# Kernel tuning notes

Hardware: AMD Instinct MI355X
Metric: run time of the kernel (lower is better)

## Reference

```python
import jax, jax.numpy as jnp
import numpy as np

N = 50000          # nodes
E_RAND = 800000    # random edges (avg degree 16)
D_IN = 128
H = 4              # heads (both layers)
C = 64             # per-head channels (both layers)
NEG_SLOPE = 0.2    # PyG GATConv default leaky_relu slope


def _gat_conv(x, src, dst, W, att_src, att_dst, bias, concat):
    """PyG GATConv (dropout=0, self-loops already in edge list).
    x:[N,Din] W:[Din,H*C] att_*:[H,C] bias:[H*C] or [C]."""
    n = x.shape[0]
    h = (x @ W).reshape(n, H, C)                      # [N,H,C]
    a_src = jnp.sum(h * att_src, axis=-1)             # [N,H]
    a_dst = jnp.sum(h * att_dst, axis=-1)             # [N,H]
    e = jax.nn.leaky_relu(a_src[src] + a_dst[dst], NEG_SLOPE)  # [E,H]
    # segment softmax over incoming edges of each destination node
    m = jax.ops.segment_max(e, dst, num_segments=n)    # [N,H]
    e = jnp.exp(e - m[dst])
    denom = jax.ops.segment_sum(e, dst, num_segments=n)
    alpha = e / (denom[dst] + 1e-16)                   # [E,H]
    msg = h[src] * alpha[..., None]                    # [E,H,C]
    out = jax.ops.segment_sum(msg, dst, num_segments=n)  # [N,H,C]
    if concat:
        out = out.reshape(n, H * C)
    else:
        out = out.mean(axis=1)
    return out + bias


def setup_inputs() -> dict:
    key = jax.random.key(0)
    ks = jax.random.split(key, 10)
    x = jax.random.normal(ks[0], (N, D_IN), jnp.float32)
    src = jax.random.randint(ks[1], (E_RAND,), 0, N)
    dst = jax.random.randint(ks[2], (E_RAND,), 0, N)
    loops = jnp.arange(N)  # add_self_loops=True (PyG default)
    edge_index = jnp.stack([jnp.concatenate([src, loops]),
                            jnp.concatenate([dst, loops])]).astype(jnp.int32)
    g = lambda k, shp, fan: (jax.random.normal(k, shp, jnp.float32) / np.float32(np.sqrt(fan)))
    W1 = g(ks[3], (D_IN, H * C), D_IN)
    att_src1 = g(ks[4], (H, C), C)
    att_dst1 = g(ks[5], (H, C), C)
    b1 = jnp.zeros((H * C,), jnp.float32)
    W2 = g(ks[6], (H * C, H * C), H * C)
    att_src2 = g(ks[7], (H, C), C)
    att_dst2 = g(ks[8], (H, C), C)
    b2 = jnp.zeros((C,), jnp.float32)
    return {"x": x, "edge_index": edge_index,
            "W1": W1, "att_src1": att_src1, "att_dst1": att_dst1, "b1": b1,
            "W2": W2, "att_src2": att_src2, "att_dst2": att_dst2, "b2": b2}


def reference(x, edge_index, W1, att_src1, att_dst1, b1, W2, att_src2, att_dst2, b2):
    src, dst = edge_index[0], edge_index[1]
    h = jax.nn.relu(_gat_conv(x, src, dst, W1, att_src1, att_dst1, b1, concat=True))
    h = jax.nn.relu(_gat_conv(h, src, dst, W2, att_src2, att_dst2, b2, concat=False))
    return jax.nn.softmax(h, axis=1)
```

## Files before the change

### kernel.cpp

```cpp
#include <hip/hip_runtime.h>


typedef __attribute__((ext_vector_type(8))) short short8;
typedef __attribute__((ext_vector_type(4))) float f32x4;
typedef __attribute__((ext_vector_type(2))) float f32x2;

static __device__ __forceinline__ ushort f2bf(float f) {
  uint u = __float_as_uint(f);
  return (ushort)((u + 0x7FFFu + ((u >> 16) & 1u)) >> 16);
}
static __device__ __forceinline__ float bf2f(ushort s) {
  return __uint_as_float(((uint)s) << 16);
}
static __device__ __forceinline__ unsigned char f2fp8(float f) {
  int p = __builtin_amdgcn_cvt_pk_fp8_f32(f, f, 0, false);
  return (unsigned char)(p & 0xFF);
}
static __device__ __forceinline__ uint4 cvt8bf(const float4& a, const float4& b) {
  uint4 hh;
  hh.x = (uint)f2bf(a.x) | ((uint)f2bf(a.y) << 16);
  hh.y = (uint)f2bf(a.z) | ((uint)f2bf(a.w) << 16);
  hh.z = (uint)f2bf(b.x) | ((uint)f2bf(b.y) << 16);
  hh.w = (uint)f2bf(b.z) | ((uint)f2bf(b.w) << 16);
  return hh;
}
static __device__ __forceinline__ void gl16(const ushort* g, ushort* l) {
  __builtin_amdgcn_global_load_lds(
      (const __attribute__((address_space(1))) uint*)(g),
      (__attribute__((address_space(3))) uint*)(l), 16, 0, 0);
}

__global__ __launch_bounds__(256)
void k_prep_hist(const float* __restrict__ W1, const float* __restrict__ W2,
                 ushort* __restrict__ w1th, ushort* __restrict__ w1tl,
                 ushort* __restrict__ w2th, ushort* __restrict__ w2tl,
                 const int* __restrict__ dstv, int* __restrict__ cnt,
                 int* __restrict__ pe, int E,
                 const float* __restrict__ x, ushort* __restrict__ xb,
                 int ng ) {
  const int b = blockIdx.x;
  const int eb = (E + 255) >> 8;
  if (b < 128) {
    int gid = b * 256 + threadIdx.x;
    int c = gid & 255, k = gid >> 8;
    float w = W1[(size_t)k * 256 + c];
    ushort h = f2bf(w);
    w1th[(size_t)c * 128 + k] = h;
    w1tl[(size_t)c * 128 + k] = f2bf(w - bf2f(h));
  } else if (b < 384) {
    int gid = (b - 128) * 256 + threadIdx.x;
    int c = gid & 255, k = gid >> 8;
    float w = W2[(size_t)k * 256 + c];
    ushort h = f2bf(w);
    w2th[(size_t)c * 256 + k] = h;
    w2tl[(size_t)c * 256 + k] = f2bf(w - bf2f(h));
  } else if (b < 384 + eb) {
    int i = (b - 384) * 256 + threadIdx.x;
    if (i < E) pe[i] = atomicAdd(&cnt[dstv[i]], 1);
  } else {
    int i = (b - 384 - eb) * 256 + threadIdx.x;
    if (i < ng) {
      const float4* xp = (const float4*)x + (size_t)i * 2;
      float4 a = xp[0], bb = xp[1];
      ((uint4*)xb)[i] = cvt8bf(a, bb);
    }
  }
}

__global__ __launch_bounds__(256)
void k_scan(const int* __restrict__ cnt, int* __restrict__ rowptr,
            int* __restrict__ bsum, int* __restrict__ bflag, int N, int E) {
  __shared__ int sm[256];
  __shared__ int s_prev;
  const int b = blockIdx.x, tid = threadIdx.x;
  const int gid = b * 256 + tid;
  int v = (gid < N) ? cnt[gid] : 0;
  sm[tid] = v;
  __syncthreads();
  for (int off = 1; off < 256; off <<= 1) {
    int t = (tid >= off) ? sm[tid - off] : 0;
    __syncthreads();
    sm[tid] += t;
    __syncthreads();
  }
  if (tid == 255) {
    atomicExch(&bsum[b], sm[255]);
    __threadfence();
    atomicExch(&bflag[b], 1);
  }
  if (tid == 0) s_prev = 0;
  __syncthreads();
  if (tid < b) {
    while (atomicAdd(&bflag[tid], 0) == 0) {}
    atomicAdd(&s_prev, atomicAdd(&bsum[tid], 0));
  }
  __syncthreads();
  if (gid < N) rowptr[gid] = s_prev + sm[tid] - v;
  if (gid == 0) rowptr[N] = E;
}

template <int K>
static __device__ __forceinline__
void gemm_body(int bid, const ushort* __restrict__ Ah,
               const ushort* __restrict__ Bth, const ushort* __restrict__ Btl,
               unsigned char* __restrict__ hout, int Nrows,
               const float* __restrict__ att_s, const float* __restrict__ att_d,
               float* __restrict__ a_s, float* __restrict__ a_d) {
  __shared__ ushort Asb[2][128][32];
  __shared__ ushort Bhb[2][128][32];
  __shared__ ushort Blb[2][128][32];

  const int nrb = (Nrows + 127) >> 7;
  const int rb = (bid >> 4) * 8 + (bid & 7);
  const int ch = (bid >> 3) & 1;
  if (rb >= nrb) return;
  const int row0 = rb * 128;
  const int col0 = ch * 128;

  const int t = threadIdx.x;
  const int lane = t & 63;
  const int w = t >> 6;
  const int wr = (w >> 1) * 64;
  const int wc = (w & 1) * 64;
  const int fr = lane & 15;
  const int fq = lane >> 4;

  const int srow = lane >> 2;
  const int skc = (lane & 3) * 8;
  int ar0 = row0 + w * 32 + srow;
  int ar1 = ar0 + 16;
  ar0 = ar0 < Nrows ? ar0 : Nrows - 1;
  ar1 = ar1 < Nrows ? ar1 : Nrows - 1;
  const ushort* agp0 = Ah + (size_t)ar0 * K + skc;
  const ushort* agp1 = Ah + (size_t)ar1 * K + skc;
  const ushort* bhg0 = Bth + (size_t)(col0 + w * 32 + srow) * K + skc;
  const ushort* bhg1 = bhg0 + (size_t)16 * K;
  const ushort* blg0 = Btl + (size_t)(col0 + w * 32 + srow) * K + skc;
  const ushort* blg1 = blg0 + (size_t)16 * K;

  f32x4 acc[4][4] = {};

  auto stage = [&](int buf, int k0) {
    gl16(agp0 + k0, &Asb[buf][w * 32][0]);
    gl16(agp1 + k0, &Asb[buf][w * 32 + 16][0]);
    gl16(bhg0 + k0, &Bhb[buf][w * 32][0]);
    gl16(bhg1 + k0, &Bhb[buf][w * 32 + 16][0]);
    gl16(blg0 + k0, &Blb[buf][w * 32][0]);
    gl16(blg1 + k0, &Blb[buf][w * 32 + 16][0]);
  };

  stage(0, 0);
  const int NK = K / 32;
#pragma unroll
  for (int ks = 0; ks < NK; ks++) {
    const int buf = ks & 1;
    __syncthreads();
    if (ks + 1 < NK) stage(buf ^ 1, (ks + 1) * 32);

    short8 fa[4], fbh[4], fbl[4];
#pragma unroll
    for (int r = 0; r < 4; r++)
      fa[r] = *(const short8*)(&Asb[buf][wr + r * 16 + fr][fq * 8]);
#pragma unroll
    for (int c = 0; c < 4; c++) {
      fbh[c] = *(const short8*)(&Bhb[buf][wc + c * 16 + fr][fq * 8]);
      fbl[c] = *(const short8*)(&Blb[buf][wc + c * 16 + fr][fq * 8]);
    }
#pragma unroll
    for (int r = 0; r < 4; r++)
#pragma unroll
      for (int c = 0; c < 4; c++) {
        acc[r][c] = __builtin_amdgcn_mfma_f32_16x16x32_bf16(fa[r], fbh[c], acc[r][c], 0, 0, 0);
        acc[r][c] = __builtin_amdgcn_mfma_f32_16x16x32_bf16(fa[r], fbl[c], acc[r][c], 0, 0, 0);
      }
  }

#pragma unroll
  for (int r = 0; r < 4; r++)
#pragma unroll
    for (int c = 0; c < 4; c++) {
      int colg = col0 + wc + c * 16 + fr;
#pragma unroll
      for (int reg = 0; reg < 4; reg++) {
        int gr = row0 + wr + r * 16 + fq * 4 + reg;
        if (gr < Nrows)
          hout[(size_t)gr * 256 + colg] = f2fp8(acc[r][c][reg]);
      }
    }

  const int head = (col0 + wc) >> 6;
  float asv[4], adv[4];
#pragma unroll
  for (int c = 0; c < 4; c++) {
    asv[c] = att_s[col0 + wc + c * 16 + fr];
    adv[c] = att_d[col0 + wc + c * 16 + fr];
  }
#pragma unroll
  for (int r = 0; r < 4; r++)
#pragma unroll
    for (int reg = 0; reg < 4; reg++) {
      float ps = 0.f, pd = 0.f;
#pragma unroll
      for (int c = 0; c < 4; c++) {
        ps += acc[r][c][reg] * asv[c];
        pd += acc[r][c][reg] * adv[c];
      }
      ps += __shfl_xor(ps, 1); pd += __shfl_xor(pd, 1);
      ps += __shfl_xor(ps, 2); pd += __shfl_xor(pd, 2);
      ps += __shfl_xor(ps, 4); pd += __shfl_xor(pd, 4);
      ps += __shfl_xor(ps, 8); pd += __shfl_xor(pd, 8);
      if (fr == 0) {
        int gr = row0 + wr + r * 16 + fq * 4 + reg;
        if (gr < Nrows) {
          a_s[(size_t)gr * 4 + head] = ps;
          a_d[(size_t)gr * 4 + head] = pd;
        }
      }
    }
}

__global__ __launch_bounds__(256)
void k_gemm1_scatter(const ushort* __restrict__ xb,
                     const ushort* __restrict__ Bth,
                     const ushort* __restrict__ Btl,
                     unsigned char* __restrict__ hout, int Nrows,
                     const float* __restrict__ att_s,
                     const float* __restrict__ att_d,
                     float* __restrict__ a_s, float* __restrict__ a_d,
                     const int* __restrict__ srcv, const int* __restrict__ dstv,
                     const int* __restrict__ rowptr, const int* __restrict__ pe,
                     int* __restrict__ col, int E, int gemm_blocks) {
  if ((int)blockIdx.x < gemm_blocks) {
    gemm_body<128>(blockIdx.x, xb, Bth, Btl, hout, Nrows,
                   att_s, att_d, a_s, a_d);
  } else {
    int base = ((int)blockIdx.x - gemm_blocks) * 1024 + threadIdx.x;
#pragma unroll
    for (int k = 0; k < 4; k++) {
      int i = base + k * 256;
      if (i < E) col[rowptr[dstv[i]] + pe[i]] = srcv[i] << 8;
    }
  }
}

__global__ __launch_bounds__(256)
void k_gemm2(const ushort* __restrict__ Ah,
             const ushort* __restrict__ Bth, const ushort* __restrict__ Btl,
             unsigned char* __restrict__ hout, int Nrows,
             const float* __restrict__ att_s, const float* __restrict__ att_d,
             float* __restrict__ a_s, float* __restrict__ a_d) {
  gemm_body<256>(blockIdx.x, Ah, Bth, Btl, hout, Nrows,
                 att_s, att_d, a_s, a_d);
}

template <int LAYER>
__global__ __launch_bounds__(256)
void k_aggr(const unsigned char* __restrict__ hsrc,
            const int* __restrict__ rowptr, const int* __restrict__ col,
            const float* __restrict__ a_s, const float* __restrict__ a_d,
            const float* __restrict__ bias,
            ushort* __restrict__ out_h, float* __restrict__ outp, int N) {
  __shared__ int   s_sh[4][64];
  __shared__ float w_sh[4][256];
  const int wv = threadIdx.x >> 6;
  const int lane = threadIdx.x & 63;
  const int node = blockIdx.x * 4 + wv;
  if (node >= N) return;
  const int hd = lane >> 4;
  const int beg = rowptr[node], end = rowptr[node + 1];
  const float4 adst = *(const float4*)(a_d + (size_t)node * 4);

  f32x2 accA = {0.f, 0.f};
  f32x2 accB = {0.f, 0.f};
  float wsum = 0.f;
  const char* hbase = (const char*)hsrc + lane * 4;

  for (int c0 = beg; c0 < end; c0 += 64) {
    int nc = min(64, end - c0);
    int off = 0;
    float4 w4 = make_float4(0.f, 0.f, 0.f, 0.f);
    if (lane < nc) {
      off = col[c0 + lane];
      const float4 a = *(const float4*)((const char*)a_s + (size_t)((uint)off >> 4));
      float e0 = a.x + adst.x; e0 = e0 > 0.f ? e0 : 0.2f * e0;
      float e1 = a.y + adst.y; e1 = e1 > 0.f ? e1 : 0.2f * e1;
      float e2 = a.z + adst.z; e2 = e2 > 0.f ? e2 : 0.2f * e2;
      float e3 = a.w + adst.w; e3 = e3 > 0.f ? e3 : 0.2f * e3;
      w4 = make_float4(__expf(e0), __expf(e1), __expf(e2), __expf(e3));
    }
    s_sh[wv][lane] = off;
    *(float4*)(&w_sh[wv][lane * 4]) = w4;
    asm volatile("s_waitcnt lgkmcnt(0)" ::: "memory");

    const float* wrow = &w_sh[wv][hd];
    const int*   srow = &s_sh[wv][0];
    int j = 0;
    for (; j + 8 <= nc; j += 8) {
      int o0 = srow[j],     o1 = srow[j + 1], o2 = srow[j + 2], o3 = srow[j + 3];
      int o4 = srow[j + 4], o5 = srow[j + 5], o6 = srow[j + 6], o7 = srow[j + 7];
      float ww0 = wrow[4 * j],      ww1 = wrow[4 * j + 4];
      float ww2 = wrow[4 * j + 8],  ww3 = wrow[4 * j + 12];
      float ww4 = wrow[4 * j + 16], ww5 = wrow[4 * j + 20];
      float ww6 = wrow[4 * j + 24], ww7 = wrow[4 * j + 28];
      uint p0 = *(const uint*)(hbase + (size_t)(uint)o0);
      uint p1 = *(const uint*)(hbase + (size_t)(uint)o1);
      uint p2 = *(const uint*)(hbase + (size_t)(uint)o2);
      uint p3 = *(const uint*)(hbase + (size_t)(uint)o3);
      uint p4 = *(const uint*)(hbase + (size_t)(uint)o4);
      uint p5 = *(const uint*)(hbase + (size_t)(uint)o5);
      uint p6 = *(const uint*)(hbase + (size_t)(uint)o6);
      uint p7 = *(const uint*)(hbase + (size_t)(uint)o7);
      wsum += ww0 + ww1 + ww2 + ww3;
      wsum += ww4 + ww5 + ww6 + ww7;
      f32x2 W;
#define EDGE_FMA(ww, p)                                                     \
      {                                                                     \
        f32x2 lo = __builtin_amdgcn_cvt_pk_f32_fp8((p), false);             \
        f32x2 hi = __builtin_amdgcn_cvt_pk_f32_fp8((p), true);              \
        W.x = (ww); W.y = (ww);                                             \
        accA = __builtin_elementwise_fma(W, lo, accA);                      \
        accB = __builtin_elementwise_fma(W, hi, accB);                      \
      }
      EDGE_FMA(ww0, p0) EDGE_FMA(ww1, p1) EDGE_FMA(ww2, p2) EDGE_FMA(ww3, p3)
      EDGE_FMA(ww4, p4) EDGE_FMA(ww5, p5) EDGE_FMA(ww6, p6) EDGE_FMA(ww7, p7)
    }
    for (; j + 4 <= nc; j += 4) {
      int o0 = srow[j], o1 = srow[j + 1], o2 = srow[j + 2], o3 = srow[j + 3];
      float ww0 = wrow[4 * j],     ww1 = wrow[4 * j + 4];
      float ww2 = wrow[4 * j + 8], ww3 = wrow[4 * j + 12];
      uint p0 = *(const uint*)(hbase + (size_t)(uint)o0);
      uint p1 = *(const uint*)(hbase + (size_t)(uint)o1);
      uint p2 = *(const uint*)(hbase + (size_t)(uint)o2);
      uint p3 = *(const uint*)(hbase + (size_t)(uint)o3);
      wsum += ww0 + ww1 + ww2 + ww3;
      f32x2 W;
      EDGE_FMA(ww0, p0) EDGE_FMA(ww1, p1) EDGE_FMA(ww2, p2) EDGE_FMA(ww3, p3)
    }
    for (; j < nc; j++) {
      int o = srow[j];
      float ww = wrow[4 * j];
      uint p = *(const uint*)(hbase + (size_t)(uint)o);
      wsum += ww;
      f32x2 W;
      EDGE_FMA(ww, p)
    }
#undef EDGE_FMA
  }

  float inv = 1.0f / wsum;
  float4 v = make_float4(accA.x * inv, accA.y * inv, accB.x * inv, accB.y * inv);

  if (LAYER == 1) {
    const float4 bv = *(const float4*)(bias + lane * 4);
    v.x = fmaxf(v.x + bv.x, 0.f);
    v.y = fmaxf(v.y + bv.y, 0.f);
    v.z = fmaxf(v.z + bv.z, 0.f);
    v.w = fmaxf(v.w + bv.w, 0.f);
    ushort4 h;
    h.x = f2bf(v.x); h.y = f2bf(v.y); h.z = f2bf(v.z); h.w = f2bf(v.w);
    *(ushort4*)(out_h + (size_t)node * 256 + lane * 4) = h;
  } else {
    v.x += __shfl_xor(v.x, 16); v.y += __shfl_xor(v.y, 16);
    v.z += __shfl_xor(v.z, 16); v.w += __shfl_xor(v.w, 16);
    v.x += __shfl_xor(v.x, 32); v.y += __shfl_xor(v.y, 32);
    v.z += __shfl_xor(v.z, 32); v.w += __shfl_xor(v.w, 32);
    const int c4 = (lane & 15) * 4;
    const float4 bv = *(const float4*)(bias + c4);
    v.x = fmaxf(v.x * 0.25f + bv.x, 0.f);
    v.y = fmaxf(v.y * 0.25f + bv.y, 0.f);
    v.z = fmaxf(v.z * 0.25f + bv.z, 0.f);
    v.w = fmaxf(v.w * 0.25f + bv.w, 0.f);
    float mx = fmaxf(fmaxf(v.x, v.y), fmaxf(v.z, v.w));
    for (int off = 8; off >= 1; off >>= 1) mx = fmaxf(mx, __shfl_xor(mx, off));
    v.x = __expf(v.x - mx); v.y = __expf(v.y - mx);
    v.z = __expf(v.z - mx); v.w = __expf(v.w - mx);
    float sum = v.x + v.y + v.z + v.w;
    for (int off = 8; off >= 1; off >>= 1) sum += __shfl_xor(sum, off);
    float is = 1.0f / sum;
    v.x *= is; v.y *= is; v.z *= is; v.w *= is;
    if (lane < 16) *(float4*)(outp + (size_t)node * 64 + c4) = v;
  }
}


extern "C" void kernel_launch(void* const* d_in, const int* in_sizes, int n_in,
                              void* d_out, int out_size, void* d_ws, size_t ws_size,
                              hipStream_t stream) {
  const float* x   = (const float*)d_in[0];
  const int*   ei  = (const int*)d_in[1];
  const float* W1  = (const float*)d_in[2];
  const float* as1 = (const float*)d_in[3];
  const float* ad1 = (const float*)d_in[4];
  const float* b1  = (const float*)d_in[5];
  const float* W2  = (const float*)d_in[6];
  const float* as2 = (const float*)d_in[7];
  const float* ad2 = (const float*)d_in[8];
  const float* b2  = (const float*)d_in[9];
  float* out = (float*)d_out;

  const int N = in_sizes[0] / 128;
  const int E = in_sizes[1] / 2;
  const int* srcv = ei;
  const int* dstv = ei + E;

  unsigned char* h8 = (unsigned char*)d_ws;
  ushort* hb   = (ushort*)(h8 + (size_t)N * 256);
  ushort* w1th = hb + (size_t)N * 256;
  ushort* w1tl = w1th + 256 * 128;
  ushort* w2th = w1tl + 256 * 128;
  ushort* w2tl = w2th + 256 * 256;
  float*  zbuf = (float*)(w2tl + 256 * 256);
  float* a_s1 = zbuf;
  float* a_d1 = a_s1 + (size_t)N * 4;
  float* a_s2 = a_d1 + (size_t)N * 4;
  float* a_d2 = a_s2 + (size_t)N * 4;
  int* rowptr = (int*)(zbuf + (size_t)N * 16);
  int* cnt    = rowptr + (N + 4);
  int* bflag  = cnt + N;
  int* bsum   = bflag + 256;
  int* pe     = bsum + 256;
  int* colx   = pe + E;
  ushort* xb  = (ushort*)(colx + E);

  const int nb = (N + 255) / 256;
  const int eb = (E + 255) / 256;
  const int eb4 = (E + 1023) / 1024;
  const int ng = N * 16;
  const int xcb = (ng + 255) / 256;

  const int nrb = (N + 127) / 128;
  const int gemm_blocks = ((nrb + 7) / 8) * 16;
  const int wb = (N + 3) / 4;

  hipMemsetAsync(cnt, 0, ((size_t)N + 256) * 4, stream);
  k_prep_hist<<<384 + eb + xcb, 256, 0, stream>>>(
      W1, W2, w1th, w1tl, w2th, w2tl, dstv, cnt, pe, E, x, xb, ng);
  k_scan<<<nb, 256, 0, stream>>>(cnt, rowptr, bsum, bflag, N, E);
  k_gemm1_scatter<<<gemm_blocks + eb4, 256, 0, stream>>>(
      xb, w1th, w1tl, h8, N, as1, ad1, a_s1, a_d1,
      srcv, dstv, rowptr, pe, colx, E, gemm_blocks);
  k_aggr<1><<<wb, 256, 0, stream>>>(h8, rowptr, colx, a_s1, a_d1, b1,
                                    hb, nullptr, N);
  k_gemm2<<<gemm_blocks, 256, 0, stream>>>(hb, w2th, w2tl, h8, N,
                                           as2, ad2, a_s2, a_d2);
  k_aggr<2><<<wb, 256, 0, stream>>>(h8, rowptr, colx, a_s2, a_d2, b2,
                                    nullptr, out, N);
}
```

Baseline: 271.5 us.

## Move degree histogram into GEMM1 launch and split CSR scatter into own kernel

Measured after the change: 270.4 us. No clear change (-0.4%).

```diff
diff --git a/kernel.cpp b/kernel.cpp
--- a/kernel.cpp
+++ b/kernel.cpp
@@ -31,15 +31,12 @@
 }
 
 __global__ __launch_bounds__(256)
-void k_prep_hist(const float* __restrict__ W1, const float* __restrict__ W2,
-                 ushort* __restrict__ w1th, ushort* __restrict__ w1tl,
-                 ushort* __restrict__ w2th, ushort* __restrict__ w2tl,
-                 const int* __restrict__ dstv, int* __restrict__ cnt,
-                 int* __restrict__ pe, int E,
-                 const float* __restrict__ x, ushort* __restrict__ xb,
-                 int ng ) {
+void k_prep(const float* __restrict__ W1, const float* __restrict__ W2,
+            ushort* __restrict__ w1th, ushort* __restrict__ w1tl,
+            ushort* __restrict__ w2th, ushort* __restrict__ w2tl,
+            const float* __restrict__ x, ushort* __restrict__ xb,
+            int ng ) {
   const int b = blockIdx.x;
-  const int eb = (E + 255) >> 8;
   if (b < 128) {
     int gid = b * 256 + threadIdx.x;
     int c = gid & 255, k = gid >> 8;
@@ -54,11 +51,8 @@
     ushort h = f2bf(w);
     w2th[(size_t)c * 256 + k] = h;
     w2tl[(size_t)c * 256 + k] = f2bf(w - bf2f(h));
-  } else if (b < 384 + eb) {
+  } else {
     int i = (b - 384) * 256 + threadIdx.x;
-    if (i < E) pe[i] = atomicAdd(&cnt[dstv[i]], 1);
-  } else {
-    int i = (b - 384 - eb) * 256 + threadIdx.x;
     if (i < ng) {
       const float4* xp = (const float4*)x + (size_t)i * 2;
       float4 a = xp[0], bb = xp[1];
@@ -220,16 +214,15 @@
 }
 
 __global__ __launch_bounds__(256)
-void k_gemm1_scatter(const ushort* __restrict__ xb,
-                     const ushort* __restrict__ Bth,
-                     const ushort* __restrict__ Btl,
-                     unsigned char* __restrict__ hout, int Nrows,
-                     const float* __restrict__ att_s,
-                     const float* __restrict__ att_d,
-                     float* __restrict__ a_s, float* __restrict__ a_d,
-                     const int* __restrict__ srcv, const int* __restrict__ dstv,
-                     const int* __restrict__ rowptr, const int* __restrict__ pe,
-                     int* __restrict__ col, int E, int gemm_blocks) {
+void k_gemm1_hist(const ushort* __restrict__ xb,
+                  const ushort* __restrict__ Bth,
+                  const ushort* __restrict__ Btl,
+                  unsigned char* __restrict__ hout, int Nrows,
+                  const float* __restrict__ att_s,
+                  const float* __restrict__ att_d,
+                  float* __restrict__ a_s, float* __restrict__ a_d,
+                  const int* __restrict__ dstv, int* __restrict__ cnt,
+                  int* __restrict__ pe, int E, int gemm_blocks) {
   if ((int)blockIdx.x < gemm_blocks) {
     gemm_body<128>(blockIdx.x, xb, Bth, Btl, hout, Nrows,
                    att_s, att_d, a_s, a_d);
@@ -238,8 +231,20 @@
 #pragma unroll
     for (int k = 0; k < 4; k++) {
       int i = base + k * 256;
-      if (i < E) col[rowptr[dstv[i]] + pe[i]] = srcv[i] << 8;
-    }
+      if (i < E) pe[i] = atomicAdd(&cnt[dstv[i]], 1);
+    }
+  }
+}
+
+__global__ __launch_bounds__(256)
+void k_scatter(const int* __restrict__ srcv, const int* __restrict__ dstv,
+               const int* __restrict__ rowptr, const int* __restrict__ pe,
+               int* __restrict__ col, int E) {
+  int base = (int)blockIdx.x * 1024 + threadIdx.x;
+#pragma unroll
+  for (int k = 0; k < 4; k++) {
+    int i = base + k * 256;
+    if (i < E) col[rowptr[dstv[i]] + pe[i]] = srcv[i] << 8;
   }
 }
 
@@ -423,7 +428,6 @@
   ushort* xb  = (ushort*)(colx + E);
 
   const int nb = (N + 255) / 256;
-  const int eb = (E + 255) / 256;
   const int eb4 = (E + 1023) / 1024;
   const int ng = N * 16;
   const int xcb = (ng + 255) / 256;
@@ -433,12 +437,13 @@
   const int wb = (N + 3) / 4;
 
   hipMemsetAsync(cnt, 0, ((size_t)N + 256) * 4, stream);
-  k_prep_hist<<<384 + eb + xcb, 256, 0, stream>>>(
-      W1, W2, w1th, w1tl, w2th, w2tl, dstv, cnt, pe, E, x, xb, ng);
+  k_prep<<<384 + xcb, 256, 0, stream>>>(W1, W2, w1th, w1tl, w2th, w2tl,
+                                        x, xb, ng);
+  k_gemm1_hist<<<gemm_blocks + eb4, 256, 0, stream>>>(
+      xb, w1th, w1tl, h8, N, as1, ad1, a_s1, a_d1,
+      dstv, cnt, pe, E, gemm_blocks);
   k_scan<<<nb, 256, 0, stream>>>(cnt, rowptr, bsum, bflag, N, E);
-  k_gemm1_scatter<<<gemm_blocks + eb4, 256, 0, stream>>>(
-      xb, w1th, w1tl, h8, N, as1, ad1, a_s1, a_d1,
-      srcv, dstv, rowptr, pe, colx, E, gemm_blocks);
+  k_scatter<<<eb4, 256, 0, stream>>>(srcv, dstv, rowptr, pe, colx, E);
   k_aggr<1><<<wb, 256, 0, stream>>>(h8, rowptr, colx, a_s1, a_d1, b1,
                                     hb, nullptr, N);
   k_gemm2<<<gemm_blocks, 256, 0, stream>>>(hb, w2th, w2tl, h8, N,
```
